# Kernel optimization log

Hardware: AMD Instinct MI355X
Metric: run time of the kernel (lower is better)

## Reference

```python
import jax, jax.numpy as jnp
import numpy as np

N_NODES = 10000
N_EDGES = 160000
C = 128          # hidden_channels
H = 8            # heads
G = 16           # groups
L_LAYERS = 5
NUM_FEAT = 14
DIM_OUT = 16
CH = C // H      # channels per head (16)


def setup_inputs() -> dict:
    key = jax.random.key(0)
    ks = jax.random.split(key, 12)
    inp = {
        "x": jax.random.normal(ks[0], (N_NODES, NUM_FEAT), dtype=jnp.float32),
        "edge_index": jax.random.randint(ks[1], (2, N_EDGES), 0, N_NODES, dtype=jnp.int64),
        "lin1_w": jax.random.normal(ks[2], (NUM_FEAT, C), dtype=jnp.float32) * 0.1,
        "lin1_b": jax.random.normal(ks[3], (C,), dtype=jnp.float32) * 0.1,
        "Wq": jax.random.normal(ks[4], (L_LAYERS, G, C // G, C // G), dtype=jnp.float32) * 0.1,
        "bq": jax.random.normal(ks[5], (L_LAYERS, C), dtype=jnp.float32) * 0.1,
        "Wk": jax.random.normal(ks[6], (L_LAYERS, G, C // G, C // G), dtype=jnp.float32) * 0.1,
        "bk": jax.random.normal(ks[7], (L_LAYERS, C), dtype=jnp.float32) * 0.1,
        "Wv": jax.random.normal(ks[8], (L_LAYERS, G, C // G, C // G), dtype=jnp.float32) * 0.1,
        "bv": jax.random.normal(ks[9], (L_LAYERS, C), dtype=jnp.float32) * 0.1,
        "lin2_w": jax.random.normal(ks[10], (C, DIM_OUT), dtype=jnp.float32) * 0.1,
        "lin2_b": jax.random.normal(ks[11], (DIM_OUT,), dtype=jnp.float32) * 0.1,
    }
    return inp


def _grouped_linear(z, W, b):
    # z: [..., C]; W: [G, C/G, C/G]; b: [C]  (PyG grouped Linear)
    lead = z.shape[:-1]
    zg = z.reshape(lead + (G, C // G))
    out = jnp.einsum('...gi,gio->...go', zg, W)
    return out.reshape(lead + (C,)) + b


def _dna_forward(x, edge_index, lin1_w, lin1_b, Wq, bq, Wk, bk, Wv, bv, lin2_w, lin2_b):
    n = x.shape[0]
    # gcn_norm with self-loops (edge_weight = 1)
    loops = jnp.arange(n, dtype=edge_index.dtype)
    row = jnp.concatenate([edge_index[0], loops])  # sources (x_j)
    col = jnp.concatenate([edge_index[1], loops])  # targets (x_i, aggregation)
    ew = jnp.ones(row.shape[0], dtype=x.dtype)
    deg = jax.ops.segment_sum(ew, col, num_segments=n)
    dis = jax.lax.rsqrt(deg)  # deg >= 1 due to self-loops
    norm = dis[row] * dis[col]  # [Et]

    h = jax.nn.relu(x @ lin1_w + lin1_b)  # [N, C]
    x_all = h[:, None, :]                  # [N, 1, C]

    scale = 1.0 / np.sqrt(CH).astype(np.float32)
    for l in range(L_LAYERS):
        q = _grouped_linear(x_all[col, -1], Wq[l], bq[l])   # [Et, C]
        k = _grouped_linear(x_all[row], Wk[l], bk[l])       # [Et, L, C]
        v = _grouped_linear(x_all[row], Wv[l], bv[l])       # [Et, L, C]
        Et, Lh = k.shape[0], k.shape[1]
        qh = q.reshape(Et, H, CH)
        kh = k.reshape(Et, Lh, H, CH)
        vh = v.reshape(Et, Lh, H, CH)
        score = jnp.einsum('ehc,elhc->ehl', qh, kh) * scale
        attn = jax.nn.softmax(score, axis=-1)
        out = jnp.einsum('ehl,elhc->ehc', attn, vh).reshape(Et, C)
        msg = norm[:, None] * out
        agg = jax.ops.segment_sum(msg, col, num_segments=n)  # [N, C]
        xl = jax.nn.relu(agg)
        x_all = jnp.concatenate([x_all, xl[:, None, :]], axis=1)

    return x_all[:, -1] @ lin2_w + lin2_b  # [N, dim]


def reference(x, edge_index, lin1_w, lin1_b, Wq, bq, Wk, bk, Wv, bv, lin2_w, lin2_b):
    return _dna_forward(x, edge_index, lin1_w, lin1_b, Wq, bq, Wk, bk, Wv, bv,
                        lin2_w, lin2_b)
```

## Files before the change

kernel.cpp:

```cpp
#include <hip/hip_runtime.h>

#define N_NODES 10000
#define N_EDGESN 160000
#define E_TOT   (N_EDGESN + N_NODES)
#define C 128
#define H 8
#define G 16
#define LLAYERS 5
#define NUM_FEAT 14
#define DIM_OUT 16
#define CH 16
#define CG 8
#define X16STRIDE (6*C)

typedef _Float16 half8 __attribute__((ext_vector_type(8)));

__global__ __launch_bounds__(256) void k_lin1(const float* __restrict__ x,
                                              const float* __restrict__ w,
                                              const float* __restrict__ b,
                                              _Float16* __restrict__ x16,
                                              int* __restrict__ counts) {
    __shared__ float sw[NUM_FEAT * C];
    __shared__ float sb[C];
    int tid = threadIdx.x;
    int gid = blockIdx.x * 256 + tid;
    if (gid < N_NODES) counts[gid] = 0;
    for (int i = tid; i < NUM_FEAT * C; i += 256) sw[i] = w[i];
    if (tid < C) sb[tid] = b[tid];
    __syncthreads();
    int node = blockIdx.x * 2 + tid / C;
    int c = tid & (C - 1);
    if (node >= N_NODES) return;
    const float* xr = x + node * NUM_FEAT;
    float acc = sb[c];
#pragma unroll
    for (int f = 0; f < NUM_FEAT; f++) acc += xr[f] * sw[f * C + c];
    acc = fmaxf(acc, 0.0f);
    x16[(size_t)node * X16STRIDE + c] = (_Float16)acc;
}

__global__ void k_count(const int* __restrict__ col, int* __restrict__ counts) {
    int e = blockIdx.x * blockDim.x + threadIdx.x;
    if (e < N_EDGESN) atomicAdd(&counts[col[e]], 1);
}

__global__ __launch_bounds__(1024) void k_scan(const int* __restrict__ counts,
                                               int* __restrict__ offs, int* __restrict__ cursor,
                                               float* __restrict__ dis,
                                               int* __restrict__ bucket_cur) {
    __shared__ int part[1024];
    __shared__ int hist[256];
    const int CHK = (N_NODES + 1023) / 1024;
    int t = threadIdx.x;
    if (t < 256) hist[t] = 0;
    __syncthreads();
    int base = t * CHK;
    int loc[CHK];
    int sum = 0;
#pragma unroll
    for (int i = 0; i < CHK; i++) {
        int idx = base + i;
        int v = (idx < N_NODES) ? (counts[idx] + 1) : 0;
        loc[i] = sum;
        sum += v;
        if (idx < N_NODES) atomicAdd(&hist[min(v, 255)], 1);
    }
    part[t] = sum;
    __syncthreads();
    for (int off = 1; off < 1024; off <<= 1) {
        int v = (t >= off) ? part[t - off] : 0;
        __syncthreads();
        part[t] += v;
        __syncthreads();
    }
    int prev = (t > 0) ? part[t - 1] : 0;
#pragma unroll
    for (int i = 0; i < CHK; i++) {
        int idx = base + i;
        if (idx < N_NODES) {
            int o = prev + loc[i];
            offs[idx] = o;
            cursor[idx] = o;
            dis[idx] = rsqrtf((float)(counts[idx] + 1));
        }
    }
    if (t == 1023) offs[N_NODES] = part[1023];
    __syncthreads();
    if (t == 0) {
        int acc = 0;
        for (int d2 = 255; d2 >= 0; d2--) { int h = hist[d2]; hist[d2] = acc; acc += h; }
    }
    __syncthreads();
    if (t < 256) bucket_cur[t] = hist[t];
}

__global__ void k_scatter(const int* __restrict__ row, const int* __restrict__ col,
                          const float* __restrict__ dis, const int* __restrict__ counts,
                          int* __restrict__ cursor, int2* __restrict__ csr,
                          int* __restrict__ bucket_cur, int* __restrict__ perm) {
    int e = blockIdx.x * blockDim.x + threadIdx.x;
    if (e < N_NODES) {
        int deg = min(counts[e] + 1, 255);
        int pos = atomicAdd(&bucket_cur[deg], 1);
        perm[pos] = e;
    }
    if (e >= E_TOT) return;
    int r = (e < N_EDGESN) ? row[e] : (e - N_EDGESN);
    int c = (e < N_EDGESN) ? col[e] : (e - N_EDGESN);
    int pos = atomicAdd(&cursor[c], 1);
    int2 pay;
    pay.x = r;
    pay.y = __float_as_int(dis[r]);
    csr[pos] = pay;
}

template <int NL>
__global__ __launch_bounds__(256) void k_attn_fly(const int* __restrict__ offs,
                                                  const int2* __restrict__ csr,
                                                  const float* __restrict__ dis,
                                                  const int* __restrict__ perm,
                                                  const float* __restrict__ Wq, const float* __restrict__ bq,
                                                  const float* __restrict__ Wk, const float* __restrict__ bk,
                                                  const float* __restrict__ Wv, const float* __restrict__ bv,
                                                  _Float16* __restrict__ x16) {
    const int l = NL - 1;
    __shared__ float red[4][C];
    __shared__ float redn[4];
    int w = threadIdx.x >> 6;
    int lane = threadIdx.x & 63;
    int nsel = w >> 1;
    int w2 = w & 1;
    int d = perm[blockIdx.x * 2 + nsel];
    int g = lane >> 2;
    int j4 = lane & 3;

    float y8[8];
    float z = 0.f;
    if constexpr (NL > 1) {
        half8 hq = *(const half8*)(x16 + (size_t)d * X16STRIDE + l * C + 8 * g);
        float xdv[8];
#pragma unroll
        for (int i = 0; i < 8; i++) xdv[i] = (float)hq[i];
        const float* bqg = bq + l * C + 8 * g;
        float4 qa = *(const float4*)bqg;
        float4 qb = *(const float4*)(bqg + 4);
        const float* wq = Wq + l * (G * CG * CG) + g * (CG * CG);
#pragma unroll
        for (int i = 0; i < 8; i++) {
            float4 ra = *(const float4*)(wq + i * CG);
            float4 rb = *(const float4*)(wq + i * CG + 4);
            qa.x += xdv[i] * ra.x; qa.y += xdv[i] * ra.y;
            qa.z += xdv[i] * ra.z; qa.w += xdv[i] * ra.w;
            qb.x += xdv[i] * rb.x; qb.y += xdv[i] * rb.y;
            qb.z += xdv[i] * rb.z; qb.w += xdv[i] * rb.w;
        }
        const float* wk = Wk + l * (G * CG * CG) + g * (CG * CG);
#pragma unroll
        for (int j = 0; j < 8; j++) {
            float4 ra = *(const float4*)(wk + j * CG);
            float4 rb = *(const float4*)(wk + j * CG + 4);
            y8[j] = qa.x * ra.x + qa.y * ra.y + qa.z * ra.z + qa.w * ra.w
                  + qb.x * rb.x + qb.y * rb.y + qb.z * rb.z + qb.w * rb.w;
        }
        const float* bkg = bk + l * C + 8 * g;
        float4 ba = *(const float4*)bkg;
        float4 bb = *(const float4*)(bkg + 4);
        z = qa.x * ba.x + qa.y * ba.y + qa.z * ba.z + qa.w * ba.w
          + qb.x * bb.x + qb.y * bb.y + qb.z * bb.z + qb.w * bb.w;
    }

    const float disd = dis[d];
    const int p0 = offs[d], p1 = offs[d + 1];
    const float scale = 0.25f;
    float xacc[8] = {0.f, 0.f, 0.f, 0.f, 0.f, 0.f, 0.f, 0.f};
    float nsum = 0.f;
    const int s0 = w2 * 4 + j4;

    if constexpr (NL == 1) {
        for (int p = p0 + s0; p < p1; p += 8) {
            int2 pay = csr[p];
            float nrm = disd * __int_as_float(pay.y);
            half8 hv = *(const half8*)(x16 + (size_t)pay.x * X16STRIDE + 8 * g);
#pragma unroll
            for (int i = 0; i < 8; i++) xacc[i] += nrm * (float)hv[i];
            nsum += nrm;
        }
    } else {
        auto consume = [&](int2 pay, const half8 (&buf)[NL]) {
            float nrm = disd * __int_as_float(pay.y);
            float xv[NL][8];
            float sc[NL];
#pragma unroll
            for (int t = 0; t < NL; t++) {
#pragma unroll
                for (int i = 0; i < 8; i++) xv[t][i] = (float)buf[t][i];
                float part = z;
#pragma unroll
                for (int i = 0; i < 8; i++) part += xv[t][i] * y8[i];
                part += __shfl_xor(part, 4);
                sc[t] = part * scale;
            }
            float mx = sc[0];
#pragma unroll
            for (int t = 1; t < NL; t++) mx = fmaxf(mx, sc[t]);
            float s = 0.f;
            float ex[8] = {0.f, 0.f, 0.f, 0.f, 0.f, 0.f, 0.f, 0.f};
#pragma unroll
            for (int t = 0; t < NL; t++) {
                float e = __expf(sc[t] - mx);
                s += e;
#pragma unroll
                for (int i = 0; i < 8; i++) ex[i] += e * xv[t][i];
            }
            float inv = nrm * __builtin_amdgcn_rcpf(s);
#pragma unroll
            for (int i = 0; i < 8; i++) xacc[i] += inv * ex[i];
            nsum += nrm;
        };

        int p = p0 + s0;
        if (p < p1) {
            int2 payA = csr[p];
            half8 bufA[NL];
            {
                const _Float16* xs = x16 + (size_t)payA.x * X16STRIDE + 8 * g;
#pragma unroll
                for (int t = 0; t < NL; t++) bufA[t] = *(const half8*)(xs + t * C);
            }
            int pn = p + 8;
            int2 payB = csr[(pn < p1) ? pn : p];
            for (; pn < p1; pn += 8) {
                half8 bufB[NL];
                const _Float16* xs = x16 + (size_t)payB.x * X16STRIDE + 8 * g;
#pragma unroll
                for (int t = 0; t < NL; t++) bufB[t] = *(const half8*)(xs + t * C);
                int pc = pn + 8;
                int2 payC = csr[(pc < p1) ? pc : p0];
                consume(payA, bufA);
                payA = payB;
                payB = payC;
#pragma unroll
                for (int t = 0; t < NL; t++) bufA[t] = bufB[t];
            }
            consume(payA, bufA);
        }
    }

#pragma unroll
    for (int i = 0; i < 8; i++) {
        xacc[i] += __shfl_xor(xacc[i], 1);
        xacc[i] += __shfl_xor(xacc[i], 2);
    }
    nsum += __shfl_xor(nsum, 1);
    nsum += __shfl_xor(nsum, 2);

    if (j4 == 0) {
#pragma unroll
        for (int i = 0; i < 8; i++) red[w][8 * g + i] = xacc[i];
    }
    if (lane == 0) redn[w] = nsum;
    __syncthreads();

    {
        int ns2 = threadIdx.x >> 7;
        int c = threadIdx.x & 127;
        int dd = perm[blockIdx.x * 2 + ns2];
        float ns = redn[2 * ns2] + redn[2 * ns2 + 1];
        int gg = c >> 3, oo = c & 7;
        const float* wv = Wv + l * (G * CG * CG) + gg * (CG * CG);
        float acc = bv[l * C + c] * ns;
#pragma unroll
        for (int i = 0; i < 8; i++)
            acc += (red[2 * ns2][8 * gg + i] + red[2 * ns2 + 1][8 * gg + i]) * wv[i * CG + oo];
        acc = fmaxf(acc, 0.f);
        x16[(size_t)dd * X16STRIDE + (l + 1) * C + c] = (_Float16)acc;
    }
}

__global__ __launch_bounds__(256) void k_lin2(const _Float16* __restrict__ x16,
                                              const float* __restrict__ w,
                                              const float* __restrict__ b,
                                              float* __restrict__ out) {
    __shared__ float sw[C * DIM_OUT];
    __shared__ float sb[DIM_OUT];
    __shared__ float sx[16][C];
    int tid = threadIdx.x;
    for (int i = tid; i < C * DIM_OUT; i += 256) sw[i] = w[i];
    if (tid < DIM_OUT) sb[tid] = b[tid];
    int node0 = blockIdx.x * 16;
    {
        int nn = node0 + (tid >> 4);
        int co = (tid & 15) * 8;
        if (nn < N_NODES) {
            half8 hv = *(const half8*)(x16 + (size_t)nn * X16STRIDE + 5 * C + co);
#pragma unroll
            for (int i = 0; i < 8; i++) sx[tid >> 4][co + i] = (float)hv[i];
        } else {
#pragma unroll
            for (int i = 0; i < 8; i++) sx[tid >> 4][co + i] = 0.f;
        }
    }
    __syncthreads();
    int node = node0 + tid / DIM_OUT;
    int o = tid & (DIM_OUT - 1);
    if (node >= N_NODES) return;
    float acc = sb[o];
    const float* xr = sx[tid / DIM_OUT];
#pragma unroll 8
    for (int c = 0; c < C; c++) acc += xr[c] * sw[c * DIM_OUT + o];
    out[node * DIM_OUT + o] = acc;
}

extern "C" void kernel_launch(void* const* d_in, const int* in_sizes, int n_in,
                              void* d_out, int out_size, void* d_ws, size_t ws_size,
                              hipStream_t stream) {
    const float* x      = (const float*)d_in[0];
    const int*   edge   = (const int*)d_in[1];
    const int*   row    = edge;
    const int*   col    = edge + N_EDGESN;
    const float* lin1_w = (const float*)d_in[2];
    const float* lin1_b = (const float*)d_in[3];
    const float* Wq     = (const float*)d_in[4];
    const float* bq     = (const float*)d_in[5];
    const float* Wk     = (const float*)d_in[6];
    const float* bk     = (const float*)d_in[7];
    const float* Wv     = (const float*)d_in[8];
    const float* bv     = (const float*)d_in[9];
    const float* lin2_w = (const float*)d_in[10];
    const float* lin2_b = (const float*)d_in[11];
    float* outp = (float*)d_out;

    _Float16* x16   = (_Float16*)d_ws;
    int2*     csr   = (int2*)(x16 + (size_t)N_NODES * X16STRIDE);
    float*    dis   = (float*)(csr + E_TOT);
    int*   counts = (int*)(dis + N_NODES);
    int*   offs   = counts + N_NODES;
    int*   cursor = offs + N_NODES + 1;
    int*   bucket_cur = cursor + N_NODES;
    int*   perm   = bucket_cur + 256;

    k_lin1<<<N_NODES / 2, 256, 0, stream>>>(x, lin1_w, lin1_b, x16, counts);
    k_count<<<(N_EDGESN + 255) / 256, 256, 0, stream>>>(col, counts);
    k_scan<<<1, 1024, 0, stream>>>(counts, offs, cursor, dis, bucket_cur);
    k_scatter<<<(E_TOT + 255) / 256, 256, 0, stream>>>(row, col, dis, counts, cursor, csr, bucket_cur, perm);

    const int ablocks = N_NODES / 2;
    for (int l = 0; l < LLAYERS; l++) {
        switch (l) {
            case 0: k_attn_fly<1><<<ablocks, 256, 0, stream>>>(offs, csr, dis, perm, Wq, bq, Wk, bk, Wv, bv, x16); break;
            case 1: k_attn_fly<2><<<ablocks, 256, 0, stream>>>(offs, csr, dis, perm, Wq, bq, Wk, bk, Wv, bv, x16); break;
            case 2: k_attn_fly<3><<<ablocks, 256, 0, stream>>>(offs, csr, dis, perm, Wq, bq, Wk, bk, Wv, bv, x16); break;
            case 3: k_attn_fly<4><<<ablocks, 256, 0, stream>>>(offs, csr, dis, perm, Wq, bq, Wk, bk, Wv, bv, x16); break;
            case 4: k_attn_fly<5><<<ablocks, 256, 0, stream>>>(offs, csr, dis, perm, Wq, bq, Wk, bk, Wv, bv, x16); break;
        }
    }
    k_lin2<<<(N_NODES + 15) / 16, 256, 0, stream>>>(x16, lin2_w, lin2_b, outp);
}
```

Before: 281.6 us.

## Use one node per attention block, fuse lin2 into last layer, parallel bucket scan

Each attention block now handles a single destination node with four waves splitting its edges (stride 16) instead of two nodes with two waves each. The grid doubles to N_NODES blocks. The final output projection is fused into the last-layer attention kernel, which removes the separate k_lin2 launch and its reload of the final features. The serial 256-entry bucket prefix in k_scan becomes a parallel shared-memory scan. These changes add more blocks and extra syncs per node, and low-degree nodes leave many lanes idle.

```diff
diff --git a/kernel.cpp b/kernel.cpp
--- a/kernel.cpp
+++ b/kernel.cpp
@@ -50,6 +50,7 @@
                                                int* __restrict__ bucket_cur) {
     __shared__ int part[1024];
     __shared__ int hist[256];
+    __shared__ int rs[256];
     const int CHK = (N_NODES + 1023) / 1024;
     int t = threadIdx.x;
     if (t < 256) hist[t] = 0;
@@ -85,13 +86,15 @@
         }
     }
     if (t == 1023) offs[N_NODES] = part[1023];
-    __syncthreads();
-    if (t == 0) {
-        int acc = 0;
-        for (int d2 = 255; d2 >= 0; d2--) { int h = hist[d2]; hist[d2] = acc; acc += h; }
-    }
-    __syncthreads();
-    if (t < 256) bucket_cur[t] = hist[t];
+    if (t < 256) rs[t] = hist[255 - t];
+    __syncthreads();
+    for (int off = 1; off < 256; off <<= 1) {
+        int v = (t < 256 && t >= off) ? rs[t - off] : 0;
+        __syncthreads();
+        if (t < 256) rs[t] += v;
+        __syncthreads();
+    }
+    if (t < 256) bucket_cur[255 - t] = rs[t] - hist[255 - t];
 }
 
 __global__ void k_scatter(const int* __restrict__ row, const int* __restrict__ col,
@@ -122,15 +125,16 @@
                                                   const float* __restrict__ Wq, const float* __restrict__ bq,
                                                   const float* __restrict__ Wk, const float* __restrict__ bk,
                                                   const float* __restrict__ Wv, const float* __restrict__ bv,
-                                                  _Float16* __restrict__ x16) {
+                                                  _Float16* __restrict__ x16,
+                                                  const float* __restrict__ lin2_w,
+                                                  const float* __restrict__ lin2_b,
+                                                  float* __restrict__ outp) {
     const int l = NL - 1;
     __shared__ float red[4][C];
     __shared__ float redn[4];
+    int d = perm[blockIdx.x];
     int w = threadIdx.x >> 6;
     int lane = threadIdx.x & 63;
-    int nsel = w >> 1;
-    int w2 = w & 1;
-    int d = perm[blockIdx.x * 2 + nsel];
     int g = lane >> 2;
     int j4 = lane & 3;
 
@@ -174,10 +178,9 @@
     const float scale = 0.25f;
     float xacc[8] = {0.f, 0.f, 0.f, 0.f, 0.f, 0.f, 0.f, 0.f};
     float nsum = 0.f;
-    const int s0 = w2 * 4 + j4;
 
     if constexpr (NL == 1) {
-        for (int p = p0 + s0; p < p1; p += 8) {
+        for (int p = p0 + 4 * w + j4; p < p1; p += 16) {
             int2 pay = csr[p];
             float nrm = disd * __int_as_float(pay.y);
             half8 hv = *(const half8*)(x16 + (size_t)pay.x * X16STRIDE + 8 * g);
@@ -218,7 +221,7 @@
             nsum += nrm;
         };
 
-        int p = p0 + s0;
+        int p = p0 + 4 * w + j4;
         if (p < p1) {
             int2 payA = csr[p];
             half8 bufA[NL];
@@ -227,14 +230,14 @@
 #pragma unroll
                 for (int t = 0; t < NL; t++) bufA[t] = *(const half8*)(xs + t * C);
             }
-            int pn = p + 8;
+            int pn = p + 16;
             int2 payB = csr[(pn < p1) ? pn : p];
-            for (; pn < p1; pn += 8) {
+            for (; pn < p1; pn += 16) {
                 half8 bufB[NL];
                 const _Float16* xs = x16 + (size_t)payB.x * X16STRIDE + 8 * g;
 #pragma unroll
                 for (int t = 0; t < NL; t++) bufB[t] = *(const half8*)(xs + t * C);
-                int pc = pn + 8;
+                int pc = pn + 16;
                 int2 payC = csr[(pc < p1) ? pc : p0];
                 consume(payA, bufA);
                 payA = payB;
@@ -260,55 +263,44 @@
     }
     if (lane == 0) redn[w] = nsum;
     __syncthreads();
-
+    if (threadIdx.x < C) {
+        int c = threadIdx.x;
+        red[0][c] = red[0][c] + red[1][c] + red[2][c] + red[3][c];
+    }
+    __syncthreads();
+    float accv = 0.f;
     {
-        int ns2 = threadIdx.x >> 7;
         int c = threadIdx.x & 127;
-        int dd = perm[blockIdx.x * 2 + ns2];
-        float ns = redn[2 * ns2] + redn[2 * ns2 + 1];
         int gg = c >> 3, oo = c & 7;
+        float ns = redn[0] + redn[1] + redn[2] + redn[3];
         const float* wv = Wv + l * (G * CG * CG) + gg * (CG * CG);
         float acc = bv[l * C + c] * ns;
 #pragma unroll
-        for (int i = 0; i < 8; i++)
-            acc += (red[2 * ns2][8 * gg + i] + red[2 * ns2 + 1][8 * gg + i]) * wv[i * CG + oo];
-        acc = fmaxf(acc, 0.f);
-        x16[(size_t)dd * X16STRIDE + (l + 1) * C + c] = (_Float16)acc;
-    }
-}
-
-__global__ __launch_bounds__(256) void k_lin2(const _Float16* __restrict__ x16,
-                                              const float* __restrict__ w,
-                                              const float* __restrict__ b,
-                                              float* __restrict__ out) {
-    __shared__ float sw[C * DIM_OUT];
-    __shared__ float sb[DIM_OUT];
-    __shared__ float sx[16][C];
-    int tid = threadIdx.x;
-    for (int i = tid; i < C * DIM_OUT; i += 256) sw[i] = w[i];
-    if (tid < DIM_OUT) sb[tid] = b[tid];
-    int node0 = blockIdx.x * 16;
-    {
-        int nn = node0 + (tid >> 4);
-        int co = (tid & 15) * 8;
-        if (nn < N_NODES) {
-            half8 hv = *(const half8*)(x16 + (size_t)nn * X16STRIDE + 5 * C + co);
-#pragma unroll
-            for (int i = 0; i < 8; i++) sx[tid >> 4][co + i] = (float)hv[i];
-        } else {
-#pragma unroll
-            for (int i = 0; i < 8; i++) sx[tid >> 4][co + i] = 0.f;
-        }
-    }
-    __syncthreads();
-    int node = node0 + tid / DIM_OUT;
-    int o = tid & (DIM_OUT - 1);
-    if (node >= N_NODES) return;
-    float acc = sb[o];
-    const float* xr = sx[tid / DIM_OUT];
-#pragma unroll 8
-    for (int c = 0; c < C; c++) acc += xr[c] * sw[c * DIM_OUT + o];
-    out[node * DIM_OUT + o] = acc;
+        for (int i = 0; i < 8; i++) acc += red[0][8 * gg + i] * wv[i * CG + oo];
+        accv = fmaxf(acc, 0.f);
+    }
+    if constexpr (NL < LLAYERS) {
+        if (threadIdx.x < C)
+            x16[(size_t)d * X16STRIDE + (l + 1) * C + threadIdx.x] = (_Float16)accv;
+    } else {
+        __syncthreads();
+        if (threadIdx.x < C) red[1][threadIdx.x] = accv;
+        __syncthreads();
+        if (threadIdx.x < 128) {
+            int o = threadIdx.x >> 3;
+            int q = threadIdx.x & 7;
+            float part = 0.f;
+#pragma unroll
+            for (int i = 0; i < 16; i++) {
+                int c = q * 16 + i;
+                part += red[1][c] * lin2_w[c * DIM_OUT + o];
+            }
+            part += __shfl_xor(part, 1);
+            part += __shfl_xor(part, 2);
+            part += __shfl_xor(part, 4);
+            if (q == 0) outp[d * DIM_OUT + o] = part + lin2_b[o];
+        }
+    }
 }
 
 extern "C" void kernel_launch(void* const* d_in, const int* in_sizes, int n_in,
@@ -344,15 +336,13 @@
     k_scan<<<1, 1024, 0, stream>>>(counts, offs, cursor, dis, bucket_cur);
     k_scatter<<<(E_TOT + 255) / 256, 256, 0, stream>>>(row, col, dis, counts, cursor, csr, bucket_cur, perm);
 
-    const int ablocks = N_NODES / 2;
     for (int l = 0; l < LLAYERS; l++) {
         switch (l) {
-            case 0: k_attn_fly<1><<<ablocks, 256, 0, stream>>>(offs, csr, dis, perm, Wq, bq, Wk, bk, Wv, bv, x16); break;
-            case 1: k_attn_fly<2><<<ablocks, 256, 0, stream>>>(offs, csr, dis, perm, Wq, bq, Wk, bk, Wv, bv, x16); break;
-            case 2: k_attn_fly<3><<<ablocks, 256, 0, stream>>>(offs, csr, dis, perm, Wq, bq, Wk, bk, Wv, bv, x16); break;
-            case 3: k_attn_fly<4><<<ablocks, 256, 0, stream>>>(offs, csr, dis, perm, Wq, bq, Wk, bk, Wv, bv, x16); break;
-            case 4: k_attn_fly<5><<<ablocks, 256, 0, stream>>>(offs, csr, dis, perm, Wq, bq, Wk, bk, Wv, bv, x16); break;
-        }
-    }
-    k_lin2<<<(N_NODES + 15) / 16, 256, 0, stream>>>(x16, lin2_w, lin2_b, outp);
-}
+            case 0: k_attn_fly<1><<<N_NODES, 256, 0, stream>>>(offs, csr, dis, perm, Wq, bq, Wk, bk, Wv, bv, x16, lin2_w, lin2_b, outp); break;
+            case 1: k_attn_fly<2><<<N_NODES, 256, 0, stream>>>(offs, csr, dis, perm, Wq, bq, Wk, bk, Wv, bv, x16, lin2_w, lin2_b, outp); break;
+            case 2: k_attn_fly<3><<<N_NODES, 256, 0, stream>>>(offs, csr, dis, perm, Wq, bq, Wk, bk, Wv, bv, x16, lin2_w, lin2_b, outp); break;
+            case 3: k_attn_fly<4><<<N_NODES, 256, 0, stream>>>(offs, csr, dis, perm, Wq, bq, Wk, bk, Wv, bv, x16, lin2_w, lin2_b, outp); break;
+            case 4: k_attn_fly<5><<<N_NODES, 256, 0, stream>>>(offs, csr, dis, perm, Wq, bq, Wk, bk, Wv, bv, x16, lin2_w, lin2_b, outp); break;
+        }
+    }
+}
```

Measured after the change: 359.9 us. +27.8%, slower.
